# Performance work log

Hardware: AMD Instinct MI355X
Metric: run time of the kernel (lower is better)

## Reference

```python
import jax, jax.numpy as jnp
import numpy as np

B = 256          # batch size
S_DIM = 512      # signalDimension
L_DIM = 2048     # latentDimension
SF = L_DIM // S_DIM   # scaleFactor = 4
NSIG = 50        # numSignals
LN_EPS = 1e-10


def _conv1d(x, w, b, dil=1):
    """Conv1d with reflect 'same' padding. x:(B,Cin,L) w:(Cout,Cin,K) b:(Cout,)."""
    k = w.shape[-1]
    pad = dil * (k - 1) // 2
    xp = jnp.pad(x, ((0, 0), (0, 0), (pad, pad)), mode='reflect')
    y = jax.lax.conv_general_dilated(
        xp, w, window_strides=(1,), padding='VALID', rhs_dilation=(dil,),
        dimension_numbers=('NCH', 'OIH', 'NCH'))
    return y + b[None, :, None]


def setup_inputs() -> dict:
    key = jax.random.key(0)
    ks = jax.random.split(key, 8)

    def w(k, shape, fan_in):
        return jax.random.normal(k, shape, jnp.float32) / np.float32(np.sqrt(fan_in))

    return {
        'latentData': jax.random.normal(ks[0], (B, L_DIM), jnp.float32),
        # sharedCNN: Conv1d(SF->2SF,k5,d1) SELU Conv1d(2SF->SF,k5,d2)
        'shared_w1': w(ks[1], (2 * SF, SF, 5), SF * 5),
        'shared_b1': jnp.zeros((2 * SF,), jnp.float32),
        'shared_w2': w(ks[2], (SF, 2 * SF, 5), 2 * SF * 5),
        'shared_b2': jnp.zeros((SF,), jnp.float32),
        # initialLayerNorm over signalDimension
        'ln_g': jnp.ones((S_DIM,), jnp.float32),
        'ln_b': jnp.zeros((S_DIM,), jnp.float32),
        # per-signal channelReduction_CNN stacks (stacked over NSIG):
        # Conv1d(SF->8,k7,d1) Conv1d(8->4,k5,d1) SELU Conv1d(4->2,k5,d1) Conv1d(2->1,k5,d2) SELU
        'sig_w1': w(ks[3], (NSIG, 8, SF, 7), SF * 7),
        'sig_b1': jnp.zeros((NSIG, 8), jnp.float32),
        'sig_w2': w(ks[4], (NSIG, 4, 8, 5), 8 * 5),
        'sig_b2': jnp.zeros((NSIG, 4), jnp.float32),
        'sig_w3': w(ks[5], (NSIG, 2, 4, 5), 4 * 5),
        'sig_b3': jnp.zeros((NSIG, 2), jnp.float32),
        'sig_w4': w(ks[6], (NSIG, 1, 2, 5), 2 * 5),
        'sig_b4': jnp.zeros((NSIG, 1), jnp.float32),
    }


def reference(latentData, shared_w1, shared_b1, shared_w2, shared_b2,
              ln_g, ln_b, sig_w1, sig_b1, sig_w2, sig_b2,
              sig_w3, sig_b3, sig_w4, sig_b4):
    b = latentData.shape[0]
    # (B, latentDim) -> (B, signalDim, SF) -> (B, SF, signalDim)
    x = latentData.reshape(b, S_DIM, SF).transpose(0, 2, 1)

    def shared(h):
        h = jax.nn.selu(_conv1d(h, shared_w1, shared_b1, dil=1))
        return _conv1d(h, shared_w2, shared_b2, dil=2)

    d = shared(shared(x)) + x  # two passes of sharedCNN + residual
    # LayerNorm over last axis (signalDimension), eps=1e-10
    mu = jnp.mean(d, axis=-1, keepdims=True)
    var = jnp.mean((d - mu) ** 2, axis=-1, keepdims=True)
    d = (d - mu) / jnp.sqrt(var + LN_EPS) * ln_g + ln_b

    def one_signal(w1, b1, w2, b2, w3, b3, w4, b4):
        h = _conv1d(d, w1, b1, dil=1)            # (B,8,L)
        h = jax.nn.selu(_conv1d(h, w2, b2, 1))   # (B,4,L)
        h = _conv1d(h, w3, b3, dil=1)            # (B,2,L)
        h = jax.nn.selu(_conv1d(h, w4, b4, 2))   # (B,1,L)
        return h[:, 0, :]                        # (B,L)

    # vectorize the 50-signal Python loop via vmap over stacked weights
    y = jax.vmap(one_signal)(sig_w1, sig_b1, sig_w2, sig_b2,
                             sig_w3, sig_b3, sig_w4, sig_b4)  # (NSIG,B,L)
    return y.transpose(1, 0, 2)  # (B, NSIG, signalDim)
```

## Files before the change

### kernel.cpp

```cpp
#include <hip/hip_runtime.h>
#include <math.h>

#define BB 256
#define L 512
#define NSIG 50
#define PAD 4
#define STR (L + 2 * PAD)

__device__ __forceinline__ int refl(int i) {
    if (i < 0) i = -i;
    if (i >= L) i = 2 * L - 2 - i;
    return i;
}

__device__ __forceinline__ float selu(float x) {
    const float scale = 1.0507009873554804934193349852946f;
    const float alpha = 1.6732632423543772848170429916717f;
    return x > 0.f ? scale * x : scale * alpha * (__expf(x) - 1.f);
}

__global__ __launch_bounds__(256) void shared_ln_kernel(
    const float* __restrict__ latent,
    const float* __restrict__ w1, const float* __restrict__ b1,
    const float* __restrict__ w2, const float* __restrict__ b2,
    const float* __restrict__ g,  const float* __restrict__ beta,
    float* __restrict__ D)
{
    __shared__ float xb[4][L];
    __shared__ float hb[8][L];
    __shared__ float yb[4][L];
    __shared__ float sw1[160], sb1[8], sw2[160], sb2[4];

    const int b = blockIdx.x;
    const int t = threadIdx.x;

    for (int i = t; i < 160; i += 256) { sw1[i] = w1[i]; sw2[i] = w2[i]; }
    if (t < 8) sb1[t] = b1[t];
    if (t < 4) sb2[t] = b2[t];

    const float* lp = latent + (size_t)b * 2048;
    for (int i = t; i < 2048; i += 256)
        xb[i & 3][i >> 2] = lp[i];
    __syncthreads();

    for (int pass = 0; pass < 2; ++pass) {
        const float (*src)[L] = (pass == 0) ? (const float (*)[L])xb
                                            : (const float (*)[L])yb;
        for (int idx = t; idx < 8 * L; idx += 256) {
            int co = idx >> 9, l = idx & (L - 1);
            float acc = sb1[co];
            #pragma unroll
            for (int ci = 0; ci < 4; ++ci) {
                const float* w = &sw1[(co * 4 + ci) * 5];
                #pragma unroll
                for (int k = 0; k < 5; ++k)
                    acc += w[k] * src[ci][refl(l + k - 2)];
            }
            hb[co][l] = selu(acc);
        }
        __syncthreads();
        for (int idx = t; idx < 4 * L; idx += 256) {
            int co = idx >> 9, l = idx & (L - 1);
            float acc = sb2[co];
            #pragma unroll
            for (int ci = 0; ci < 8; ++ci) {
                const float* w = &sw2[(co * 8 + ci) * 5];
                #pragma unroll
                for (int k = 0; k < 5; ++k)
                    acc += w[k] * hb[ci][refl(l + 2 * k - 4)];
            }
            if (pass == 1) acc += xb[co][l];
            yb[co][l] = acc;
        }
        __syncthreads();
    }

    const int wave = t >> 6;
    const int lane = t & 63;
    float v[8];
    float s = 0.f;
    #pragma unroll
    for (int j = 0; j < 8; ++j) { v[j] = yb[wave][lane * 8 + j]; s += v[j]; }
    #pragma unroll
    for (int off = 32; off > 0; off >>= 1) s += __shfl_down(s, off);
    s = __shfl(s, 0);
    const float mu = s * (1.f / 512.f);
    float s2 = 0.f;
    #pragma unroll
    for (int j = 0; j < 8; ++j) { float d = v[j] - mu; s2 += d * d; }
    #pragma unroll
    for (int off = 32; off > 0; off >>= 1) s2 += __shfl_down(s2, off);
    s2 = __shfl(s2, 0);
    const float rinv = rsqrtf(s2 * (1.f / 512.f) + 1e-10f);

    float* Dp = D + ((size_t)b * 4 + wave) * L;
    #pragma unroll
    for (int j = 0; j < 8; ++j) {
        int l = lane * 8 + j;
        Dp[l] = (v[j] - mu) * rinv * g[l] + beta[l];
    }
}

__global__ __launch_bounds__(256) void signal_kernel(
    const float* __restrict__ D,
    const float* __restrict__ w1, const float* __restrict__ b1,
    const float* __restrict__ w2, const float* __restrict__ b2,
    const float* __restrict__ w3, const float* __restrict__ b3,
    const float* __restrict__ w4, const float* __restrict__ b4,
    float* __restrict__ out)
{
    const int s = blockIdx.x;
    const int b = blockIdx.y;
    const int t = threadIdx.x;
    const int p0 = t * 2;

    __shared__ float bufA[4][STR];
    __shared__ float bufB[8][STR];

    {
        const float4* Dv = (const float4*)(D + (size_t)b * 4 * L);
        #pragma unroll
        for (int i = t; i < L; i += 256) {
            float4 v = Dv[i];
            int c = i >> 7, l4 = (i & 127) * 4;
            float* dst = &bufA[c][PAD + l4];
            dst[0] = v.x; dst[1] = v.y; dst[2] = v.z; dst[3] = v.w;
        }
    }
    __syncthreads();
    if (t < 4 * 8) {
        int r = t >> 3, j = t & 7;
        if (j < 4) bufA[r][PAD - 1 - j] = bufA[r][PAD + 1 + j];
        else { int i = j - 4; bufA[r][PAD + L + i] = bufA[r][PAD + L - 2 - i]; }
    }
    __syncthreads();

    {
        float x[4][8];
        #pragma unroll
        for (int ci = 0; ci < 4; ++ci)
            #pragma unroll
            for (int j = 0; j < 8; ++j)
                x[ci][j] = bufA[ci][p0 + j + (PAD - 3)];
        #pragma unroll
        for (int co = 0; co < 8; ++co) {
            float a0 = b1[s * 8 + co], a1 = a0;
            #pragma unroll
            for (int ci = 0; ci < 4; ++ci)
                #pragma unroll
                for (int k = 0; k < 7; ++k) {
                    float w = w1[((s * 8 + co) * 4 + ci) * 7 + k];
                    a0 += w * x[ci][k];
                    a1 += w * x[ci][k + 1];
                }
            bufB[co][PAD + p0] = a0;
            bufB[co][PAD + p0 + 1] = a1;
        }
    }
    __syncthreads();
    if (t < 8 * 8) {
        int r = t >> 3, j = t & 7;
        if (j < 4) bufB[r][PAD - 1 - j] = bufB[r][PAD + 1 + j];
        else { int i = j - 4; bufB[r][PAD + L + i] = bufB[r][PAD + L - 2 - i]; }
    }
    __syncthreads();

    {
        float x[8][6];
        #pragma unroll
        for (int ci = 0; ci < 8; ++ci)
            #pragma unroll
            for (int j = 0; j < 6; ++j)
                x[ci][j] = bufB[ci][p0 + j + (PAD - 2)];
        #pragma unroll
        for (int co = 0; co < 4; ++co) {
            float a0 = b2[s * 4 + co], a1 = a0;
            #pragma unroll
            for (int ci = 0; ci < 8; ++ci)
                #pragma unroll
                for (int k = 0; k < 5; ++k) {
                    float w = w2[((s * 4 + co) * 8 + ci) * 5 + k];
                    a0 += w * x[ci][k];
                    a1 += w * x[ci][k + 1];
                }
            bufA[co][PAD + p0] = selu(a0);
            bufA[co][PAD + p0 + 1] = selu(a1);
        }
    }
    __syncthreads();
    if (t < 4 * 8) {
        int r = t >> 3, j = t & 7;
        if (j < 4) bufA[r][PAD - 1 - j] = bufA[r][PAD + 1 + j];
        else { int i = j - 4; bufA[r][PAD + L + i] = bufA[r][PAD + L - 2 - i]; }
    }
    __syncthreads();

    {
        float x[4][6];
        #pragma unroll
        for (int ci = 0; ci < 4; ++ci)
            #pragma unroll
            for (int j = 0; j < 6; ++j)
                x[ci][j] = bufA[ci][p0 + j + (PAD - 2)];
        #pragma unroll
        for (int co = 0; co < 2; ++co) {
            float a0 = b3[s * 2 + co], a1 = a0;
            #pragma unroll
            for (int ci = 0; ci < 4; ++ci)
                #pragma unroll
                for (int k = 0; k < 5; ++k) {
                    float w = w3[((s * 2 + co) * 4 + ci) * 5 + k];
                    a0 += w * x[ci][k];
                    a1 += w * x[ci][k + 1];
                }
            bufB[co][PAD + p0] = a0;
            bufB[co][PAD + p0 + 1] = a1;
        }
    }
    __syncthreads();
    if (t < 2 * 8) {
        int r = t >> 3, j = t & 7;
        if (j < 4) bufB[r][PAD - 1 - j] = bufB[r][PAD + 1 + j];
        else { int i = j - 4; bufB[r][PAD + L + i] = bufB[r][PAD + L - 2 - i]; }
    }
    __syncthreads();

    {
        float x[2][10];
        #pragma unroll
        for (int ci = 0; ci < 2; ++ci)
            #pragma unroll
            for (int j = 0; j < 10; ++j)
                x[ci][j] = bufB[ci][p0 + j + (PAD - 4)];
        float a0 = b4[s], a1 = a0;
        #pragma unroll
        for (int ci = 0; ci < 2; ++ci)
            #pragma unroll
            for (int k = 0; k < 5; ++k) {
                float w = w4[(s * 2 + ci) * 5 + k];
                a0 += w * x[ci][2 * k];
                a1 += w * x[ci][2 * k + 1];
            }
        float2 r;
        r.x = selu(a0);
        r.y = selu(a1);
        *(float2*)&out[((size_t)b * NSIG + s) * L + p0] = r;
    }
}

extern "C" void kernel_launch(void* const* d_in, const int* in_sizes, int n_in,
                              void* d_out, int out_size, void* d_ws, size_t ws_size,
                              hipStream_t stream) {
    const float* latent = (const float*)d_in[0];
    const float* sw1 = (const float*)d_in[1];
    const float* sb1 = (const float*)d_in[2];
    const float* sw2 = (const float*)d_in[3];
    const float* sb2 = (const float*)d_in[4];
    const float* ln_g = (const float*)d_in[5];
    const float* ln_b = (const float*)d_in[6];
    const float* g_w1 = (const float*)d_in[7];
    const float* g_b1 = (const float*)d_in[8];
    const float* g_w2 = (const float*)d_in[9];
    const float* g_b2 = (const float*)d_in[10];
    const float* g_w3 = (const float*)d_in[11];
    const float* g_b3 = (const float*)d_in[12];
    const float* g_w4 = (const float*)d_in[13];
    const float* g_b4 = (const float*)d_in[14];
    float* out = (float*)d_out;
    float* D = (float*)d_ws;

    shared_ln_kernel<<<BB, 256, 0, stream>>>(latent, sw1, sb1, sw2, sb2,
                                             ln_g, ln_b, D);
    signal_kernel<<<dim3(NSIG, BB), 256, 0, stream>>>(D, g_w1, g_b1, g_w2, g_b2,
                                                      g_w3, g_b3, g_w4, g_b4, out);
}
```

Before: 105.6 us.

## Compute four outputs per thread in signal kernel with vectorized LDS access

```diff
diff --git a/kernel.cpp b/kernel.cpp
--- a/kernel.cpp
+++ b/kernel.cpp
@@ -101,7 +101,7 @@
     }
 }
 
-__global__ __launch_bounds__(256) void signal_kernel(
+__global__ __launch_bounds__(128) void signal_kernel(
     const float* __restrict__ D,
     const float* __restrict__ w1, const float* __restrict__ b1,
     const float* __restrict__ w2, const float* __restrict__ b2,
@@ -112,23 +112,28 @@
     const int s = blockIdx.x;
     const int b = blockIdx.y;
     const int t = threadIdx.x;
-    const int p0 = t * 2;
+    const int p0 = t * 4;
 
     __shared__ float bufA[4][STR];
     __shared__ float bufB[8][STR];
 
-    {
-        const float4* Dv = (const float4*)(D + (size_t)b * 4 * L);
-        #pragma unroll
-        for (int i = t; i < L; i += 256) {
+    const float* W1 = w1 + s * 224; const float* B1 = b1 + s * 8;
+    const float* W2 = w2 + s * 160; const float* B2 = b2 + s * 4;
+    const float* W3 = w3 + s * 40;  const float* B3 = b3 + s * 2;
+    const float* W4 = w4 + s * 10;
+
+    {
+        const float4* Dv = (const float4*)(D + (size_t)b * 2048);
+        #pragma unroll
+        for (int j = 0; j < 4; ++j) {
+            int i = t + j * 128;
             float4 v = Dv[i];
-            int c = i >> 7, l4 = (i & 127) * 4;
-            float* dst = &bufA[c][PAD + l4];
-            dst[0] = v.x; dst[1] = v.y; dst[2] = v.z; dst[3] = v.w;
-        }
-    }
-    __syncthreads();
-    if (t < 4 * 8) {
+            int c = i >> 7, col = (i & 127) << 2;
+            *(float4*)&bufA[c][PAD + col] = v;
+        }
+    }
+    __syncthreads();
+    if (t < 32) {
         int r = t >> 3, j = t & 7;
         if (j < 4) bufA[r][PAD - 1 - j] = bufA[r][PAD + 1 + j];
         else { int i = j - 4; bufA[r][PAD + L + i] = bufA[r][PAD + L - 2 - i]; }
@@ -136,29 +141,38 @@
     __syncthreads();
 
     {
-        float x[4][8];
-        #pragma unroll
-        for (int ci = 0; ci < 4; ++ci)
-            #pragma unroll
-            for (int j = 0; j < 8; ++j)
-                x[ci][j] = bufA[ci][p0 + j + (PAD - 3)];
+        float acc[8][4];
         #pragma unroll
         for (int co = 0; co < 8; ++co) {
-            float a0 = b1[s * 8 + co], a1 = a0;
-            #pragma unroll
-            for (int ci = 0; ci < 4; ++ci)
+            float bb = B1[co];
+            #pragma unroll
+            for (int pp = 0; pp < 4; ++pp) acc[co][pp] = bb;
+        }
+        #pragma unroll
+        for (int ci = 0; ci < 4; ++ci) {
+            float x[12];
+            const float* row = &bufA[ci][p0];
+            *(float4*)&x[0] = *(const float4*)&row[0];
+            *(float4*)&x[4] = *(const float4*)&row[4];
+            *(float4*)&x[8] = *(const float4*)&row[8];
+            #pragma unroll
+            for (int co = 0; co < 8; ++co)
                 #pragma unroll
                 for (int k = 0; k < 7; ++k) {
-                    float w = w1[((s * 8 + co) * 4 + ci) * 7 + k];
-                    a0 += w * x[ci][k];
-                    a1 += w * x[ci][k + 1];
+                    float w = W1[(co * 4 + ci) * 7 + k];
+                    #pragma unroll
+                    for (int pp = 0; pp < 4; ++pp)
+                        acc[co][pp] += w * x[pp + k + 1];
                 }
-            bufB[co][PAD + p0] = a0;
-            bufB[co][PAD + p0 + 1] = a1;
-        }
-    }
-    __syncthreads();
-    if (t < 8 * 8) {
+        }
+        #pragma unroll
+        for (int co = 0; co < 8; ++co) {
+            float4 v = { acc[co][0], acc[co][1], acc[co][2], acc[co][3] };
+            *(float4*)&bufB[co][PAD + p0] = v;
+        }
+    }
+    __syncthreads();
+    if (t < 64) {
         int r = t >> 3, j = t & 7;
         if (j < 4) bufB[r][PAD - 1 - j] = bufB[r][PAD + 1 + j];
         else { int i = j - 4; bufB[r][PAD + L + i] = bufB[r][PAD + L - 2 - i]; }
@@ -166,29 +180,39 @@
     __syncthreads();
 
     {
-        float x[8][6];
-        #pragma unroll
-        for (int ci = 0; ci < 8; ++ci)
-            #pragma unroll
-            for (int j = 0; j < 6; ++j)
-                x[ci][j] = bufB[ci][p0 + j + (PAD - 2)];
+        float acc[4][4];
         #pragma unroll
         for (int co = 0; co < 4; ++co) {
-            float a0 = b2[s * 4 + co], a1 = a0;
-            #pragma unroll
-            for (int ci = 0; ci < 8; ++ci)
+            float bb = B2[co];
+            #pragma unroll
+            for (int pp = 0; pp < 4; ++pp) acc[co][pp] = bb;
+        }
+        #pragma unroll
+        for (int ci = 0; ci < 8; ++ci) {
+            float x[8];
+            const float* row = &bufB[ci][p0 + 2];
+            *(float2*)&x[0] = *(const float2*)&row[0];
+            *(float4*)&x[2] = *(const float4*)&row[2];
+            *(float2*)&x[6] = *(const float2*)&row[6];
+            #pragma unroll
+            for (int co = 0; co < 4; ++co)
                 #pragma unroll
                 for (int k = 0; k < 5; ++k) {
-                    float w = w2[((s * 4 + co) * 8 + ci) * 5 + k];
-                    a0 += w * x[ci][k];
-                    a1 += w * x[ci][k + 1];
+                    float w = W2[(co * 8 + ci) * 5 + k];
+                    #pragma unroll
+                    for (int pp = 0; pp < 4; ++pp)
+                        acc[co][pp] += w * x[pp + k];
                 }
-            bufA[co][PAD + p0] = selu(a0);
-            bufA[co][PAD + p0 + 1] = selu(a1);
-        }
-    }
-    __syncthreads();
-    if (t < 4 * 8) {
+        }
+        #pragma unroll
+        for (int co = 0; co < 4; ++co) {
+            float4 v = { selu(acc[co][0]), selu(acc[co][1]),
+                         selu(acc[co][2]), selu(acc[co][3]) };
+            *(float4*)&bufA[co][PAD + p0] = v;
+        }
+    }
+    __syncthreads();
+    if (t < 32) {
         int r = t >> 3, j = t & 7;
         if (j < 4) bufA[r][PAD - 1 - j] = bufA[r][PAD + 1 + j];
         else { int i = j - 4; bufA[r][PAD + L + i] = bufA[r][PAD + L - 2 - i]; }
@@ -196,29 +220,38 @@
     __syncthreads();
 
     {
-        float x[4][6];
-        #pragma unroll
-        for (int ci = 0; ci < 4; ++ci)
-            #pragma unroll
-            for (int j = 0; j < 6; ++j)
-                x[ci][j] = bufA[ci][p0 + j + (PAD - 2)];
+        float acc[2][4];
         #pragma unroll
         for (int co = 0; co < 2; ++co) {
-            float a0 = b3[s * 2 + co], a1 = a0;
-            #pragma unroll
-            for (int ci = 0; ci < 4; ++ci)
+            float bb = B3[co];
+            #pragma unroll
+            for (int pp = 0; pp < 4; ++pp) acc[co][pp] = bb;
+        }
+        #pragma unroll
+        for (int ci = 0; ci < 4; ++ci) {
+            float x[8];
+            const float* row = &bufA[ci][p0 + 2];
+            *(float2*)&x[0] = *(const float2*)&row[0];
+            *(float4*)&x[2] = *(const float4*)&row[2];
+            *(float2*)&x[6] = *(const float2*)&row[6];
+            #pragma unroll
+            for (int co = 0; co < 2; ++co)
                 #pragma unroll
                 for (int k = 0; k < 5; ++k) {
-                    float w = w3[((s * 2 + co) * 4 + ci) * 5 + k];
-                    a0 += w * x[ci][k];
-                    a1 += w * x[ci][k + 1];
+                    float w = W3[(co * 4 + ci) * 5 + k];
+                    #pragma unroll
+                    for (int pp = 0; pp < 4; ++pp)
+                        acc[co][pp] += w * x[pp + k];
                 }
-            bufB[co][PAD + p0] = a0;
-            bufB[co][PAD + p0 + 1] = a1;
-        }
-    }
-    __syncthreads();
-    if (t < 2 * 8) {
+        }
+        #pragma unroll
+        for (int co = 0; co < 2; ++co) {
+            float4 v = { acc[co][0], acc[co][1], acc[co][2], acc[co][3] };
+            *(float4*)&bufB[co][PAD + p0] = v;
+        }
+    }
+    __syncthreads();
+    if (t < 16) {
         int r = t >> 3, j = t & 7;
         if (j < 4) bufB[r][PAD - 1 - j] = bufB[r][PAD + 1 + j];
         else { int i = j - 4; bufB[r][PAD + L + i] = bufB[r][PAD + L - 2 - i]; }
@@ -226,25 +259,27 @@
     __syncthreads();
 
     {
-        float x[2][10];
-        #pragma unroll
-        for (int ci = 0; ci < 2; ++ci)
-            #pragma unroll
-            for (int j = 0; j < 10; ++j)
-                x[ci][j] = bufB[ci][p0 + j + (PAD - 4)];
-        float a0 = b4[s], a1 = a0;
-        #pragma unroll
-        for (int ci = 0; ci < 2; ++ci)
+        float acc[4];
+        float bb = b4[s];
+        #pragma unroll
+        for (int pp = 0; pp < 4; ++pp) acc[pp] = bb;
+        #pragma unroll
+        for (int ci = 0; ci < 2; ++ci) {
+            float x[12];
+            const float* row = &bufB[ci][p0];
+            *(float4*)&x[0] = *(const float4*)&row[0];
+            *(float4*)&x[4] = *(const float4*)&row[4];
+            *(float4*)&x[8] = *(const float4*)&row[8];
             #pragma unroll
             for (int k = 0; k < 5; ++k) {
-                float w = w4[(s * 2 + ci) * 5 + k];
-                a0 += w * x[ci][2 * k];
-                a1 += w * x[ci][2 * k + 1];
+                float w = W4[ci * 5 + k];
+                #pragma unroll
+                for (int pp = 0; pp < 4; ++pp)
+                    acc[pp] += w * x[pp + 2 * k];
             }
-        float2 r;
-        r.x = selu(a0);
-        r.y = selu(a1);
-        *(float2*)&out[((size_t)b * NSIG + s) * L + p0] = r;
+        }
+        float4 r = { selu(acc[0]), selu(acc[1]), selu(acc[2]), selu(acc[3]) };
+        *(float4*)&out[((size_t)b * NSIG + s) * L + p0] = r;
     }
 }
 
@@ -271,6 +306,6 @@
 
     shared_ln_kernel<<<BB, 256, 0, stream>>>(latent, sw1, sb1, sw2, sb2,
                                              ln_g, ln_b, D);
-    signal_kernel<<<dim3(NSIG, BB), 256, 0, stream>>>(D, g_w1, g_b1, g_w2, g_b2,
+    signal_kernel<<<dim3(NSIG, BB), 128, 0, stream>>>(D, g_w1, g_b1, g_w2, g_b2,
                                                       g_w3, g_b3, g_w4, g_b4, out);
 }
```

Measured after the change: 121.3 us. 14.8% more time.
